# Kernel tuning notes

Measured on AMD Instinct MI355X. Metric: run time of the kernel, lower is better.

## Reference

```python
import jax, jax.numpy as jnp
import numpy as np

EPS = 1e-5  # BatchNorm eps
N_NODES, N_EDGES, F = 100000, 600000, 128


def setup_inputs() -> dict:
    key = jax.random.key(0)
    ks = jax.random.split(key, 16)
    inp = {
        "node_representations": jax.random.normal(ks[0], (N_NODES, F), jnp.float32),
        "edges": jax.random.randint(ks[1], (2, N_EDGES), 0, N_NODES, jnp.int64 if jax.config.jax_enable_x64 else jnp.int32),
        "edge_weights": jax.random.uniform(ks[2], (N_EDGES,), jnp.float32),
        # preprocess FFN: BatchNorm1d(F) [eval mode] + Linear(F, F) + GELU
        "pre_bn_gamma": jax.random.normal(ks[3], (F,), jnp.float32) * 0.1 + 1.0,
        "pre_bn_beta": jax.random.normal(ks[4], (F,), jnp.float32) * 0.1,
        "pre_bn_mean": jax.random.normal(ks[5], (F,), jnp.float32) * 0.1,
        "pre_bn_var": jax.random.uniform(ks[6], (F,), jnp.float32) * 0.5 + 0.5,
        "pre_w": jax.random.normal(ks[7], (F, F), jnp.float32) / np.sqrt(F),
        "pre_b": jnp.zeros((F,), jnp.float32),
        # update FFN: BatchNorm1d(2F) [eval mode] + Linear(2F, F) + GELU
        "upd_bn_gamma": jax.random.normal(ks[8], (2 * F,), jnp.float32) * 0.1 + 1.0,
        "upd_bn_beta": jax.random.normal(ks[9], (2 * F,), jnp.float32) * 0.1,
        "upd_bn_mean": jax.random.normal(ks[10], (2 * F,), jnp.float32) * 0.1,
        "upd_bn_var": jax.random.uniform(ks[11], (2 * F,), jnp.float32) * 0.5 + 0.5,
        "upd_w": jax.random.normal(ks[12], (2 * F, F), jnp.float32) / np.sqrt(2 * F),
        "upd_b": jnp.zeros((F,), jnp.float32),
    }
    return inp


def _bn_eval(x, gamma, beta, mean, var):
    return (x - mean) * (gamma / jnp.sqrt(var + EPS)) + beta


def reference(node_representations, edges, edge_weights,
              pre_bn_gamma, pre_bn_beta, pre_bn_mean, pre_bn_var, pre_w, pre_b,
              upd_bn_gamma, upd_bn_beta, upd_bn_mean, upd_bn_var, upd_w, upd_b):
    n_nodes, f = node_representations.shape
    node_idx, nbr_idx = edges[0], edges[1]
    # gather neighbour features: [E, F]
    x = node_representations[nbr_idx]
    # preprocess FFN (BN eval, dropout=identity in eval, linear, gelu)
    x = _bn_eval(x, pre_bn_gamma, pre_bn_beta, pre_bn_mean, pre_bn_var)
    x = jax.nn.gelu(x @ pre_w + pre_b, approximate=False)
    x = x * edge_weights[:, None]
    # mean aggregation (replicates torch.unique-on-expanded-indices counter = degree * F)
    agg = jax.ops.segment_sum(x, node_idx, num_segments=n_nodes)
    deg = jax.ops.segment_sum(jnp.ones_like(edge_weights), node_idx, num_segments=n_nodes)
    counter = (deg * f)[:, None]
    agg = jnp.where(counter > 0, agg / jnp.where(counter > 0, counter, 1.0), 0.0)
    # concat combine + update FFN
    emb = jnp.concatenate([node_representations, agg], axis=-1)
    emb = _bn_eval(emb, upd_bn_gamma, upd_bn_beta, upd_bn_mean, upd_bn_var)
    emb = jax.nn.gelu(emb @ upd_w + upd_b, approximate=False)
    return emb
```

## Files before the change

kernel.cpp:

```cpp
#include <hip/hip_runtime.h>
#include <math.h>

#define F 128
#define TWO_F 256
#define BN_EPS 1e-5f
#define PAD_A 136
#define PAD_A2 264

typedef unsigned short ushort_t;
typedef unsigned char uchar_t;
typedef __attribute__((ext_vector_type(8))) short bfrag;
typedef __attribute__((ext_vector_type(4))) float ffrag;
typedef __attribute__((ext_vector_type(2))) float floatx2;

__device__ __forceinline__ float gelu_exact(float x) {
    return 0.5f * x * (1.0f + erff(x * 0.70710678118654752f));
}
__device__ __forceinline__ ushort_t f2bf(float x) {
    unsigned int u = __float_as_uint(x);
    u = (u + 0x7FFFu + ((u >> 16) & 1u)) >> 16;
    return (ushort_t)u;
}
__device__ __forceinline__ unsigned int pk2(float a, float b) {
    return (unsigned int)f2bf(a) | ((unsigned int)f2bf(b) << 16);
}

__device__ __forceinline__ void fma4_fp8(float* acc, unsigned int d, float w) {
    floatx2 lo = __builtin_amdgcn_cvt_pk_f32_fp8(d, false);
    floatx2 hi = __builtin_amdgcn_cvt_pk_f32_fp8(d, true);
    acc[0] = fmaf(w, lo.x, acc[0]);
    acc[1] = fmaf(w, lo.y, acc[1]);
    acc[2] = fmaf(w, hi.x, acc[2]);
    acc[3] = fmaf(w, hi.y, acc[3]);
}
__device__ __forceinline__ void fma16_fp8(float* acc, uint4 a, float w) {
    fma4_fp8(acc + 0,  a.x, w); fma4_fp8(acc + 4,  a.y, w);
    fma4_fp8(acc + 8,  a.z, w); fma4_fp8(acc + 12, a.w, w);
}

__global__ __launch_bounds__(256) void prep(
    const float* __restrict__ pre_w, const float* __restrict__ pre_b,
    const float* __restrict__ g1, const float* __restrict__ be1,
    const float* __restrict__ m1, const float* __restrict__ v1,
    const float* __restrict__ upd_w, const float* __restrict__ upd_b,
    const float* __restrict__ g2, const float* __restrict__ be2,
    const float* __restrict__ m2, const float* __restrict__ v2,
    ushort_t* __restrict__ W1T, ushort_t* __restrict__ W2T,
    float* __restrict__ b1f, float* __restrict__ b2f,
    const int* __restrict__ edges, int* __restrict__ counts, int nEdges, int histBlocks) {
    const int t = threadIdx.x;
    if (blockIdx.x == 0) {
        __shared__ float t1[F], t2[TWO_F];
        if (t < F) {
            float s = g1[t] * rsqrtf(v1[t] + BN_EPS);
            t1[t] = be1[t] - m1[t] * s;
        }
        {
            float s = g2[t] * rsqrtf(v2[t] + BN_EPS);
            t2[t] = be2[t] - m2[t] * s;
        }
        __syncthreads();
        if (t < F) {
            float acc = pre_b[t];
            #pragma unroll 4
            for (int k = 0; k < F; ++k) acc = fmaf(t1[k], pre_w[k * F + t], acc);
            b1f[t] = acc;
        } else {
            int j = t - F;
            float acc = upd_b[j];
            #pragma unroll 4
            for (int k = 0; k < TWO_F; ++k) acc = fmaf(t2[k], upd_w[k * F + j], acc);
            b2f[j] = acc;
        }
    } else if (blockIdx.x <= 128) {
        int idx = (blockIdx.x - 1) * 256 + t;
        if (idx < F * F) {
            int k = idx & (F - 1), n = idx >> 7;
            float s = g1[k] * rsqrtf(v1[k] + BN_EPS);
            W1T[idx] = f2bf(s * pre_w[k * F + n]);
        }
        {
            int k = idx & (TWO_F - 1), n = idx >> 8;
            float s = g2[k] * rsqrtf(v2[k] + BN_EPS);
            W2T[idx] = f2bf(s * upd_w[k * F + n]);
        }
    } else {
        int b = blockIdx.x - 129;
        for (int i = b * 256 + t; i < nEdges; i += histBlocks * 256)
            atomicAdd(&counts[edges[i]], 1);
    }
}

__global__ __launch_bounds__(1024) void scan_pass1(const int* __restrict__ counts,
                                                   int* __restrict__ offsets,
                                                   int* __restrict__ blocksums, int n) {
    __shared__ int sb[1024];
    const int t = threadIdx.x;
    int idx = blockIdx.x * 1024 + t;
    int v = (idx < n) ? counts[idx] : 0;
    sb[t] = v;
    __syncthreads();
    for (int off = 1; off < 1024; off <<= 1) {
        int x = (t >= off) ? sb[t - off] : 0;
        __syncthreads();
        sb[t] += x;
        __syncthreads();
    }
    if (idx < n) offsets[idx + 1] = sb[t];
    if (t == 1023) blocksums[blockIdx.x] = sb[t];
}

__global__ __launch_bounds__(1024) void scan_pass3(const int* __restrict__ counts,
                                                   int* __restrict__ offsets,
                                                   const int* __restrict__ blocksums,
                                                   int* __restrict__ cursor, int n) {
    __shared__ int sb[1024];
    const int t = threadIdx.x;
    sb[t] = (t < blockIdx.x) ? blocksums[t] : 0;
    __syncthreads();
    #pragma unroll
    for (int off = 512; off > 0; off >>= 1) {
        if (t < off) sb[t] += sb[t + off];
        __syncthreads();
    }
    int base = sb[0];
    int idx = blockIdx.x * 1024 + t;
    if (idx < n) {
        int incl = offsets[idx + 1] + base;
        offsets[idx + 1] = incl;
        cursor[idx] = incl - counts[idx];
    }
    if (blockIdx.x == 0 && t == 0) offsets[0] = 0;
}

__global__ __launch_bounds__(256) void gemm1_fill(
    const float* __restrict__ nodes, const ushort_t* __restrict__ W1T,
    const float* __restrict__ b1f, uchar_t* __restrict__ G8, int nNodes,
    const int* __restrict__ edges, const float* __restrict__ ew,
    int* __restrict__ cursor, int2* __restrict__ csr, int nEdges,
    int gB, int fillBlocks) {
    __shared__ ushort_t As[64 * PAD_A];
    __shared__ float bs[F];
    const int t = threadIdx.x;

    if (blockIdx.x >= gB) {
        int b = blockIdx.x - gB;
        for (int e = b * 256 + t; e < nEdges; e += fillBlocks * 256) {
            int dst = edges[e];
            int pos = atomicAdd(&cursor[dst], 1);
            csr[pos] = make_int2(edges[nEdges + e], __float_as_int(ew[e]));
        }
        return;
    }

    const int base = blockIdx.x * 64;
    {
        int r = t >> 2, q = t & 3;
        int n = base + r;
        int sn = (n < nNodes) ? n : 0;
        const float4* src = reinterpret_cast<const float4*>(nodes + (size_t)sn * F + q * 32);
        uint4 pv[4];
        #pragma unroll
        for (int i = 0; i < 4; ++i) {
            float4 a = src[2 * i], b = src[2 * i + 1];
            pv[i].x = pk2(a.x, a.y); pv[i].y = pk2(a.z, a.w);
            pv[i].z = pk2(b.x, b.y); pv[i].w = pk2(b.z, b.w);
        }
        uint4* dst = reinterpret_cast<uint4*>(As + r * PAD_A + q * 32);
        #pragma unroll
        for (int i = 0; i < 4; ++i) dst[i] = pv[i];
    }
    if (t < F) bs[t] = b1f[t];
    __syncthreads();

    const int lane = t & 63, w = t >> 6;
    const int m = lane & 15, quad = lane >> 4;

    ffrag acc[8];
    #pragma unroll
    for (int c = 0; c < 8; ++c) acc[c] = (ffrag){0.f, 0.f, 0.f, 0.f};

    #pragma unroll
    for (int kk = 0; kk < 4; ++kk) {
        int k0 = kk * 32 + quad * 8;
        bfrag a = *reinterpret_cast<const bfrag*>(As + (w * 16 + m) * PAD_A + k0);
        #pragma unroll
        for (int c = 0; c < 8; ++c) {
            bfrag b = *reinterpret_cast<const bfrag*>(W1T + (size_t)(c * 16 + m) * F + k0);
            acc[c] = __builtin_amdgcn_mfma_f32_16x16x32_bf16(a, b, acc[c], 0, 0, 0);
        }
    }

    #pragma unroll
    for (int c = 0; c < 8; ++c) {
        int feat = c * 16 + m;
        float bj = bs[feat];
        #pragma unroll
        for (int i = 0; i < 4; ++i) {
            int n = base + w * 16 + quad * 4 + i;
            if (n < nNodes) {
                float v = gelu_exact(acc[c][i] + bj);
                int pkd = __builtin_amdgcn_cvt_pk_fp8_f32(v, v, 0, false);
                G8[(size_t)n * F + feat] = (uchar_t)(pkd & 0xFF);
            }
        }
    }
}

__global__ __launch_bounds__(256) void node_fused(
    const float* __restrict__ nodes, const uchar_t* __restrict__ G8,
    const int* __restrict__ offsets, const int2* __restrict__ csr,
    const ushort_t* __restrict__ W2T, const float* __restrict__ b2f,
    float* __restrict__ out, int nNodes) {
    __shared__ ushort_t As[32 * PAD_A2];
    __shared__ float bs[F];
    const int t = threadIdx.x;
    const int base = blockIdx.x * 32;
    const int r = t >> 3, q = t & 7;

    if (t < F) bs[t] = b2f[t];

    {
        int n = base + r;
        int sn = (n < nNodes) ? n : 0;
        const float4* src = reinterpret_cast<const float4*>(nodes + (size_t)sn * F + q * 16);
        uint4 pv[2];
        #pragma unroll
        for (int i = 0; i < 2; ++i) {
            float4 a = src[2 * i], b = src[2 * i + 1];
            pv[i].x = pk2(a.x, a.y); pv[i].y = pk2(a.z, a.w);
            pv[i].z = pk2(b.x, b.y); pv[i].w = pk2(b.z, b.w);
        }
        uint4* dst = reinterpret_cast<uint4*>(As + r * PAD_A2 + q * 16);
        dst[0] = pv[0]; dst[1] = pv[1];
    }

    {
        int n = base + r;
        float acc[16];
        #pragma unroll
        for (int j = 0; j < 16; ++j) acc[j] = 0.f;
        int s = 0, e = 0;
        if (n < nNodes) { s = offsets[n]; e = offsets[n + 1]; }
        int i = s;
        for (; i + 3 < e; i += 4) {
            int2 m0 = csr[i], m1 = csr[i + 1], m2 = csr[i + 2], m3 = csr[i + 3];
            uint4 a0 = *reinterpret_cast<const uint4*>(G8 + (size_t)m0.x * F + q * 16);
            uint4 a1 = *reinterpret_cast<const uint4*>(G8 + (size_t)m1.x * F + q * 16);
            uint4 a2 = *reinterpret_cast<const uint4*>(G8 + (size_t)m2.x * F + q * 16);
            uint4 a3 = *reinterpret_cast<const uint4*>(G8 + (size_t)m3.x * F + q * 16);
            fma16_fp8(acc, a0, __int_as_float(m0.y));
            fma16_fp8(acc, a1, __int_as_float(m1.y));
            fma16_fp8(acc, a2, __int_as_float(m2.y));
            fma16_fp8(acc, a3, __int_as_float(m3.y));
        }
        for (; i < e; ++i) {
            int2 m0 = csr[i];
            uint4 a0 = *reinterpret_cast<const uint4*>(G8 + (size_t)m0.x * F + q * 16);
            fma16_fp8(acc, a0, __int_as_float(m0.y));
        }
        int deg = e - s;
        float inv = (deg > 0) ? 1.0f / ((float)deg * (float)F) : 0.f;
        unsigned int* dstu = reinterpret_cast<unsigned int*>(As + r * PAD_A2 + F + q * 16);
        #pragma unroll
        for (int j = 0; j < 8; ++j) dstu[j] = pk2(acc[2 * j] * inv, acc[2 * j + 1] * inv);
    }
    __syncthreads();

    const int lane = t & 63, w = t >> 6;
    const int m = lane & 15, quad = lane >> 4;
    const int rg = w & 1, cg = w >> 1;

    ffrag acc[4];
    #pragma unroll
    for (int c = 0; c < 4; ++c) acc[c] = (ffrag){0.f, 0.f, 0.f, 0.f};

    #pragma unroll
    for (int kk = 0; kk < 8; ++kk) {
        int k0 = kk * 32 + quad * 8;
        bfrag a = *reinterpret_cast<const bfrag*>(As + (rg * 16 + m) * PAD_A2 + k0);
        #pragma unroll
        for (int c = 0; c < 4; ++c) {
            int feat = cg * 64 + c * 16 + m;
            bfrag b = *reinterpret_cast<const bfrag*>(W2T + (size_t)feat * TWO_F + k0);
            acc[c] = __builtin_amdgcn_mfma_f32_16x16x32_bf16(a, b, acc[c], 0, 0, 0);
        }
    }

    #pragma unroll
    for (int c = 0; c < 4; ++c) {
        int feat = cg * 64 + c * 16 + m;
        float bj = bs[feat];
        #pragma unroll
        for (int i = 0; i < 4; ++i) {
            int n = base + rg * 16 + quad * 4 + i;
            if (n < nNodes) out[(size_t)n * F + feat] = gelu_exact(acc[c][i] + bj);
        }
    }
}

extern "C" void kernel_launch(void* const* d_in, const int* in_sizes, int n_in,
                              void* d_out, int out_size, void* d_ws, size_t ws_size,
                              hipStream_t stream) {
    const float* nodes  = (const float*)d_in[0];
    const int*   edges  = (const int*)d_in[1];
    const float* ew     = (const float*)d_in[2];
    const float* pre_g  = (const float*)d_in[3];
    const float* pre_be = (const float*)d_in[4];
    const float* pre_m  = (const float*)d_in[5];
    const float* pre_v  = (const float*)d_in[6];
    const float* pre_w  = (const float*)d_in[7];
    const float* pre_b  = (const float*)d_in[8];
    const float* upd_g  = (const float*)d_in[9];
    const float* upd_be = (const float*)d_in[10];
    const float* upd_m  = (const float*)d_in[11];
    const float* upd_v  = (const float*)d_in[12];
    const float* upd_w  = (const float*)d_in[13];
    const float* upd_b  = (const float*)d_in[14];
    float* out = (float*)d_out;

    const int nNodes = in_sizes[0] / F;
    const int nEdges = in_sizes[2];
    const int nChunks = (nNodes + 1023) / 1024;
    const int histBlocks = 1024;
    const int gB = (nNodes + 63) / 64;
    const int fillBlocks = 1024;

    char* p = (char*)d_ws;
    int*      counts    = (int*)p;       p += (size_t)nNodes * 4;
    int*      offsets   = (int*)p;       p += (size_t)(nNodes + 4) * 4;
    int*      cursor    = (int*)p;       p += (size_t)nNodes * 4;
    int*      blocksums = (int*)p;       p += 1024 * 4;
    int2*     csr       = (int2*)p;      p += (size_t)nEdges * 8;
    float*    b1f       = (float*)p;     p += F * 4;
    float*    b2f       = (float*)p;     p += F * 4;
    ushort_t* W1T       = (ushort_t*)p;  p += F * F * 2;
    ushort_t* W2T       = (ushort_t*)p;  p += TWO_F * F * 2;
    uchar_t*  G8        = (uchar_t*)p;

    hipMemsetAsync(counts, 0, (size_t)nNodes * 4, stream);

    prep<<<129 + histBlocks, 256, 0, stream>>>(
        pre_w, pre_b, pre_g, pre_be, pre_m, pre_v,
        upd_w, upd_b, upd_g, upd_be, upd_m, upd_v,
        W1T, W2T, b1f, b2f, edges, counts, nEdges, histBlocks);

    scan_pass1<<<nChunks, 1024, 0, stream>>>(counts, offsets, blocksums, nNodes);
    scan_pass3<<<nChunks, 1024, 0, stream>>>(counts, offsets, blocksums, cursor, nNodes);

    gemm1_fill<<<gB + fillBlocks, 256, 0, stream>>>(
        nodes, W1T, b1f, G8, nNodes, edges, ew, cursor, csr, nEdges, gB, fillBlocks);

    node_fused<<<(nNodes + 31) / 32, 256, 0, stream>>>(
        nodes, G8, offsets, csr, W2T, b2f, out, nNodes);
}
```

Baseline: 299.7 us.

## Balance edge aggregation across threads with LDS atomics and row tags in CSR

The aggregation phase of node_fused now splits the block's whole edge range evenly across 32 thread-groups instead of one group per destination node, removing load imbalance from skewed degrees. The local row id is packed into the top 5 bits of the CSR source index so each group can detect row boundaries, flush partial sums into a zeroed fp32 LDS accumulator via atomicAdd, and software-prefetch the next edge. The node-feature half of the A operand is now loaded and converted straight from global memory inside the MFMA loop instead of being staged in LDS. The cost is LDS atomics and an extra LDS zeroing pass. The packing also assumes source indices fit in 27 bits.

```diff
diff --git a/kernel.cpp b/kernel.cpp
--- a/kernel.cpp
+++ b/kernel.cpp
@@ -5,7 +5,7 @@
 #define TWO_F 256
 #define BN_EPS 1e-5f
 #define PAD_A 136
-#define PAD_A2 264
+#define PAD_ACC 132
 
 typedef unsigned short ushort_t;
 typedef unsigned char uchar_t;
@@ -23,19 +23,6 @@
 }
 __device__ __forceinline__ unsigned int pk2(float a, float b) {
     return (unsigned int)f2bf(a) | ((unsigned int)f2bf(b) << 16);
-}
-
-__device__ __forceinline__ void fma4_fp8(float* acc, unsigned int d, float w) {
-    floatx2 lo = __builtin_amdgcn_cvt_pk_f32_fp8(d, false);
-    floatx2 hi = __builtin_amdgcn_cvt_pk_f32_fp8(d, true);
-    acc[0] = fmaf(w, lo.x, acc[0]);
-    acc[1] = fmaf(w, lo.y, acc[1]);
-    acc[2] = fmaf(w, hi.x, acc[2]);
-    acc[3] = fmaf(w, hi.y, acc[3]);
-}
-__device__ __forceinline__ void fma16_fp8(float* acc, uint4 a, float w) {
-    fma4_fp8(acc + 0,  a.x, w); fma4_fp8(acc + 4,  a.y, w);
-    fma4_fp8(acc + 8,  a.z, w); fma4_fp8(acc + 12, a.w, w);
 }
 
 __global__ __launch_bounds__(256) void prep(
@@ -148,7 +135,8 @@
         for (int e = b * 256 + t; e < nEdges; e += fillBlocks * 256) {
             int dst = edges[e];
             int pos = atomicAdd(&cursor[dst], 1);
-            csr[pos] = make_int2(edges[nEdges + e], __float_as_int(ew[e]));
+            int src = edges[nEdges + e];
+            csr[pos] = make_int2(src | ((dst & 31) << 27), __float_as_int(ew[e]));
         }
         return;
     }
@@ -212,77 +200,122 @@
     const int* __restrict__ offsets, const int2* __restrict__ csr,
     const ushort_t* __restrict__ W2T, const float* __restrict__ b2f,
     float* __restrict__ out, int nNodes) {
-    __shared__ ushort_t As[32 * PAD_A2];
+    __shared__ float accS[32 * PAD_ACC];
     __shared__ float bs[F];
+    __shared__ int offs[33];
     const int t = threadIdx.x;
     const int base = blockIdx.x * 32;
-    const int r = t >> 3, q = t & 7;
 
     if (t < F) bs[t] = b2f[t];
+    if (t < 33) {
+        int idx = base + t;
+        offs[t] = offsets[(idx < nNodes) ? idx : nNodes];
+    }
+    for (int i = t; i < 32 * PAD_ACC; i += 256) accS[i] = 0.f;
+    __syncthreads();
 
     {
-        int n = base + r;
-        int sn = (n < nNodes) ? n : 0;
-        const float4* src = reinterpret_cast<const float4*>(nodes + (size_t)sn * F + q * 16);
-        uint4 pv[2];
-        #pragma unroll
-        for (int i = 0; i < 2; ++i) {
-            float4 a = src[2 * i], b = src[2 * i + 1];
-            pv[i].x = pk2(a.x, a.y); pv[i].y = pk2(a.z, a.w);
-            pv[i].z = pk2(b.x, b.y); pv[i].w = pk2(b.z, b.w);
-        }
-        uint4* dst = reinterpret_cast<uint4*>(As + r * PAD_A2 + q * 16);
-        dst[0] = pv[0]; dst[1] = pv[1];
-    }
-
-    {
-        int n = base + r;
-        float acc[16];
-        #pragma unroll
-        for (int j = 0; j < 16; ++j) acc[j] = 0.f;
-        int s = 0, e = 0;
-        if (n < nNodes) { s = offsets[n]; e = offsets[n + 1]; }
-        int i = s;
-        for (; i + 3 < e; i += 4) {
-            int2 m0 = csr[i], m1 = csr[i + 1], m2 = csr[i + 2], m3 = csr[i + 3];
-            uint4 a0 = *reinterpret_cast<const uint4*>(G8 + (size_t)m0.x * F + q * 16);
-            uint4 a1 = *reinterpret_cast<const uint4*>(G8 + (size_t)m1.x * F + q * 16);
-            uint4 a2 = *reinterpret_cast<const uint4*>(G8 + (size_t)m2.x * F + q * 16);
-            uint4 a3 = *reinterpret_cast<const uint4*>(G8 + (size_t)m3.x * F + q * 16);
-            fma16_fp8(acc, a0, __int_as_float(m0.y));
-            fma16_fp8(acc, a1, __int_as_float(m1.y));
-            fma16_fp8(acc, a2, __int_as_float(m2.y));
-            fma16_fp8(acc, a3, __int_as_float(m3.y));
-        }
-        for (; i < e; ++i) {
-            int2 m0 = csr[i];
-            uint4 a0 = *reinterpret_cast<const uint4*>(G8 + (size_t)m0.x * F + q * 16);
-            fma16_fp8(acc, a0, __int_as_float(m0.y));
-        }
-        int deg = e - s;
-        float inv = (deg > 0) ? 1.0f / ((float)deg * (float)F) : 0.f;
-        unsigned int* dstu = reinterpret_cast<unsigned int*>(As + r * PAD_A2 + F + q * 16);
-        #pragma unroll
-        for (int j = 0; j < 8; ++j) dstu[j] = pk2(acc[2 * j] * inv, acc[2 * j + 1] * inv);
-    }
-    __syncthreads();
-
-    const int lane = t & 63, w = t >> 6;
+        const int eg = t >> 3, oct = t & 7;
+        const int eBeg = offs[0], eEnd = offs[32];
+        const int nE = eEnd - eBeg;
+        const int len = (nE + 31) >> 5;
+        int e = eBeg + eg * len;
+        const int eStop = min(e + len, eEnd);
+
+        float vacc[16];
+        #pragma unroll
+        for (int j = 0; j < 16; ++j) vacc[j] = 0.f;
+        int curRl = -1;
+
+        if (e < eStop) {
+            int2 mc = csr[e];
+            uint4 ac = *reinterpret_cast<const uint4*>(
+                G8 + (size_t)(((unsigned int)mc.x) & 0x07FFFFFFu) * F + oct * 16);
+            while (true) {
+                bool more = (e + 1) < eStop;
+                int2 mn;
+                uint4 an;
+                if (more) {
+                    mn = csr[e + 1];
+                    an = *reinterpret_cast<const uint4*>(
+                        G8 + (size_t)(((unsigned int)mn.x) & 0x07FFFFFFu) * F + oct * 16);
+                }
+                int rl = (int)(((unsigned int)mc.x) >> 27);
+                float w = __int_as_float(mc.y);
+                if (rl != curRl) {
+                    if (curRl >= 0) {
+                        float* rowp = accS + curRl * PAD_ACC + oct * 16;
+                        #pragma unroll
+                        for (int j = 0; j < 16; ++j) atomicAdd(&rowp[j], vacc[j]);
+                        #pragma unroll
+                        for (int j = 0; j < 16; ++j) vacc[j] = 0.f;
+                    }
+                    curRl = rl;
+                }
+                floatx2 p;
+                p = __builtin_amdgcn_cvt_pk_f32_fp8(ac.x, false); vacc[0]  = fmaf(w, p.x, vacc[0]);  vacc[1]  = fmaf(w, p.y, vacc[1]);
+                p = __builtin_amdgcn_cvt_pk_f32_fp8(ac.x, true ); vacc[2]  = fmaf(w, p.x, vacc[2]);  vacc[3]  = fmaf(w, p.y, vacc[3]);
+                p = __builtin_amdgcn_cvt_pk_f32_fp8(ac.y, false); vacc[4]  = fmaf(w, p.x, vacc[4]);  vacc[5]  = fmaf(w, p.y, vacc[5]);
+                p = __builtin_amdgcn_cvt_pk_f32_fp8(ac.y, true ); vacc[6]  = fmaf(w, p.x, vacc[6]);  vacc[7]  = fmaf(w, p.y, vacc[7]);
+                p = __builtin_amdgcn_cvt_pk_f32_fp8(ac.z, false); vacc[8]  = fmaf(w, p.x, vacc[8]);  vacc[9]  = fmaf(w, p.y, vacc[9]);
+                p = __builtin_amdgcn_cvt_pk_f32_fp8(ac.z, true ); vacc[10] = fmaf(w, p.x, vacc[10]); vacc[11] = fmaf(w, p.y, vacc[11]);
+                p = __builtin_amdgcn_cvt_pk_f32_fp8(ac.w, false); vacc[12] = fmaf(w, p.x, vacc[12]); vacc[13] = fmaf(w, p.y, vacc[13]);
+                p = __builtin_amdgcn_cvt_pk_f32_fp8(ac.w, true ); vacc[14] = fmaf(w, p.x, vacc[14]); vacc[15] = fmaf(w, p.y, vacc[15]);
+                if (!more) break;
+                mc = mn; ac = an; ++e;
+            }
+            float* rowp = accS + curRl * PAD_ACC + oct * 16;
+            #pragma unroll
+            for (int j = 0; j < 16; ++j) atomicAdd(&rowp[j], vacc[j]);
+        }
+    }
+    __syncthreads();
+
+    const int lane = t & 63, wv = t >> 6;
     const int m = lane & 15, quad = lane >> 4;
-    const int rg = w & 1, cg = w >> 1;
+    const int rg = wv & 1, cg = wv >> 1;
+    const int arow = rg * 16 + m;
+    const int deg = offs[arow + 1] - offs[arow];
+    const float inv = (deg > 0) ? 1.0f / ((float)deg * (float)F) : 0.f;
+
+    const int grow = base + arow;
+    const float4* nrow = reinterpret_cast<const float4*>(
+        nodes + (size_t)((grow < nNodes) ? grow : 0) * F);
+    const float4* arow4 = reinterpret_cast<const float4*>(accS + arow * PAD_ACC);
 
     ffrag acc[4];
     #pragma unroll
     for (int c = 0; c < 4; ++c) acc[c] = (ffrag){0.f, 0.f, 0.f, 0.f};
 
     #pragma unroll
-    for (int kk = 0; kk < 8; ++kk) {
-        int k0 = kk * 32 + quad * 8;
-        bfrag a = *reinterpret_cast<const bfrag*>(As + (rg * 16 + m) * PAD_A2 + k0);
+    for (int kk = 0; kk < 4; ++kk) {
+        int c0 = kk * 32 + quad * 8;
+        float4 f0 = nrow[kk * 8 + quad * 2];
+        float4 f1 = nrow[kk * 8 + quad * 2 + 1];
+        bfrag a;
+        unsigned int* au = reinterpret_cast<unsigned int*>(&a);
+        au[0] = pk2(f0.x, f0.y); au[1] = pk2(f0.z, f0.w);
+        au[2] = pk2(f1.x, f1.y); au[3] = pk2(f1.z, f1.w);
         #pragma unroll
         for (int c = 0; c < 4; ++c) {
             int feat = cg * 64 + c * 16 + m;
-            bfrag b = *reinterpret_cast<const bfrag*>(W2T + (size_t)feat * TWO_F + k0);
+            bfrag b = *reinterpret_cast<const bfrag*>(W2T + (size_t)feat * TWO_F + c0);
+            acc[c] = __builtin_amdgcn_mfma_f32_16x16x32_bf16(a, b, acc[c], 0, 0, 0);
+        }
+    }
+    #pragma unroll
+    for (int kk = 0; kk < 4; ++kk) {
+        int c0 = kk * 32 + quad * 8;
+        float4 f0 = arow4[kk * 8 + quad * 2];
+        float4 f1 = arow4[kk * 8 + quad * 2 + 1];
+        bfrag a;
+        unsigned int* au = reinterpret_cast<unsigned int*>(&a);
+        au[0] = pk2(f0.x * inv, f0.y * inv); au[1] = pk2(f0.z * inv, f0.w * inv);
+        au[2] = pk2(f1.x * inv, f1.y * inv); au[3] = pk2(f1.z * inv, f1.w * inv);
+        #pragma unroll
+        for (int c = 0; c < 4; ++c) {
+            int feat = cg * 64 + c * 16 + m;
+            bfrag b = *reinterpret_cast<const bfrag*>(W2T + (size_t)feat * TWO_F + 128 + c0);
             acc[c] = __builtin_amdgcn_mfma_f32_16x16x32_bf16(a, b, acc[c], 0, 0, 0);
         }
     }
```

Result: slower. 358.4 us (+19.6%).
